# Kernel optimization log

Measured on AMD Instinct MI355X. Metric: run time of the kernel, lower is better.

Reference implementation:

```python
import jax, jax.numpy as jnp
import numpy as np

B, T, N, FIN, FOUT, EDGE_DIM = 8, 16, 256, 32, 32, 16


def setup_inputs() -> dict:
    key = jax.random.key(0)
    ks = jax.random.split(key, 8)
    def xavier(k, shape):
        fan_in, fan_out = shape[0], shape[1]
        limit = float(np.sqrt(6.0 / (fan_in + fan_out)))
        return jax.random.uniform(k, shape, jnp.float32, -limit, limit)
    return {
        "x": jax.random.normal(ks[0], (B, T, N, FIN), jnp.float32),
        "adj": jax.random.uniform(ks[1], (N, N), jnp.float32),
        # edge_net: Linear(1, edge_dim) -> GELU -> Linear(edge_dim, Fin*Fout)
        "w1": xavier(ks[2], (1, EDGE_DIM)),
        "b1": jnp.zeros((EDGE_DIM,), jnp.float32),
        "w2": xavier(ks[3], (EDGE_DIM, FIN * FOUT)),
        "b2": jnp.zeros((FIN * FOUT,), jnp.float32),
        # node_lin: Linear(Fin, Fout)
        "node_w": xavier(ks[4], (FIN, FOUT)),
        "node_b": jnp.zeros((FOUT,), jnp.float32),
    }


def reference(x, adj, w1, b1, w2, b2, node_w, node_b):
    # edge-conditioned weights: (N, N, Fin, Fout)
    h = jax.nn.gelu(adj[:, :, None] * w1[0] + b1, approximate=False)  # (N,N,E)
    edge_w = (h @ w2 + b2).reshape(N, N, FIN, FOUT)
    # msg[b,t,i,j,:] = sum_f x[b,t,j,f] * edge_w[i,j,f,:]; agg = sum_j msg
    agg = jnp.einsum("btjf,ijfo->btio", x, edge_w)  # (B,T,N,Fout)
    y = jax.nn.gelu(x @ node_w + node_b + agg, approximate=False)
    return y
```

## Files before the change

kernel.cpp:

```cpp
#include <hip/hip_runtime.h>
#include <math.h>

#define NB    256
#define FINN  32
#define FOUTN 32
#define BT    128


typedef __attribute__((ext_vector_type(8))) short short8;
typedef __attribute__((ext_vector_type(4))) float floatx4;

#define MFMA16(a,b,c) __builtin_amdgcn_mfma_f32_16x16x32_bf16((a),(b),(c),0,0,0)

__device__ __forceinline__ float gelu_f(float v) {
    return 0.5f * v * (1.0f + erff(v * 0.70710678118654752f));
}
__device__ __forceinline__ ushort f2bf(float x) {
    union { float f; unsigned u; } v; v.f = x;
    unsigned r = (v.u + 0x7FFFu + ((v.u >> 16) & 1u)) >> 16;
    return (ushort)r;
}
__device__ __forceinline__ uint2 pack4(floatx4 d) {
    uint2 p;
    p.x = (unsigned)f2bf(d[0]) | ((unsigned)f2bf(d[1]) << 16);
    p.y = (unsigned)f2bf(d[2]) | ((unsigned)f2bf(d[3]) << 16);
    return p;
}

typedef __attribute__((address_space(1))) void gvoid_t;
typedef __attribute__((address_space(3))) void lvoid_t;
__device__ __forceinline__ void gload_lds16(const void* g, void* l) {
    __builtin_amdgcn_global_load_lds((gvoid_t*)g, (lvoid_t*)l, 16, 0, 0);
}

__global__ __launch_bounds__(256) void prep_kernel(
        const float* __restrict__ x,   const float* __restrict__ adj,
        const float* __restrict__ w1,  const float* __restrict__ b1,
        const float* __restrict__ w2,  const float* __restrict__ b2,
        const float* __restrict__ node_w, const float* __restrict__ node_b,
        ushort* __restrict__ Hf, ushort* __restrict__ w2f,
        ushort* __restrict__ xaf, ushort* __restrict__ nwf,
        float* __restrict__ bias2g) {
    int bid = blockIdx.x;
    int tid = threadIdx.x;

    if (bid < 128) {
        __shared__ float adjs[16][264];
        __shared__ float w1s[16], b1s[16];
        int it = bid & 15;
        int kq8 = bid >> 4;
        if (tid < 16) { w1s[tid] = w1[tid]; b1s[tid] = b1[tid]; }
        #pragma unroll
        for (int q = 0; q < 4; ++q) {
            int u = q * 256 + tid;
            int row = u >> 6, c4 = u & 63;
            *(float4*)&adjs[row][c4 * 4] =
                ((const float4*)(adj + ((size_t)it * 16 + row) * 256))[c4];
        }
        __syncthreads();
        #pragma unroll
        for (int q = 0; q < 4; ++q) {
            int u = q * 256 + tid;
            int ks = kq8 * 16 + (u >> 6);
            int lane = u & 63;
            int m = lane & 15, quad = lane >> 4;
            int e = ks >> 3;
            int j0 = (ks & 7) * 32 + quad * 8;
            float w = w1s[e], b = b1s[e];
            ushort tmp[8];
            #pragma unroll
            for (int d = 0; d < 8; ++d)
                tmp[d] = f2bf(gelu_f(adjs[m][j0 + d] * w + b));
            *(int4*)(Hf + (((size_t)it * 128 + ks) * 64 + lane) * 8) = *(int4*)tmp;
        }
        return;
    }
    if (bid < 160) {
        int wv = tid >> 6, lane = tid & 63, m = lane & 15, quad = lane >> 4;
        int bt = (bid - 128) * 4 + wv;
        #pragma unroll
        for (int jt = 0; jt < 16; ++jt) {
            const float* xs = x + ((size_t)bt * NB + jt * 16 + m) * FINN + quad * 8;
            float4 lo = *(const float4*)xs;
            float4 hi = *(const float4*)(xs + 4);
            ushort tmp[8];
            tmp[0]=f2bf(lo.x); tmp[1]=f2bf(lo.y); tmp[2]=f2bf(lo.z); tmp[3]=f2bf(lo.w);
            tmp[4]=f2bf(hi.x); tmp[5]=f2bf(hi.y); tmp[6]=f2bf(hi.z); tmp[7]=f2bf(hi.w);
            *(int4*)(xaf + (((size_t)bt * 16 + jt) * 64 + lane) * 8) = *(int4*)tmp;
        }
        return;
    }
    if (bid < 288) {
        __shared__ float Sp[8][32];
        __shared__ float Svs[32];
        int bt = bid - 160;
        int f = tid & 31, grp = tid >> 5;
        float s = 0.f;
        for (int j = grp; j < NB; j += 8)
            s += x[((size_t)bt * NB + j) * FINN + f];
        Sp[grp][f] = s;
        __syncthreads();
        if (tid < 32) {
            float s2 = 0.f;
            #pragma unroll
            for (int g = 0; g < 8; ++g) s2 += Sp[g][tid];
            Svs[tid] = s2;
        }
        __syncthreads();
        if (tid < 32) {
            float bb = node_b[tid];
            #pragma unroll
            for (int f2 = 0; f2 < FINN; ++f2)
                bb += Svs[f2] * b2[f2 * FOUTN + tid];
            bias2g[bt * 32 + tid] = bb;
        }
        return;
    }
    for (int s = 0; s < 2048; s += 256) {
        int slot = s + tid;
        int e = slot >> 7, r = slot & 127;
        int ot = r >> 6, lane = r & 63;
        int m = lane & 15, quad = lane >> 4;
        const float* src = w2 + (size_t)e * 1024 + (quad * 8) * 32 + ot * 16 + m;
        ushort tmp[8];
        #pragma unroll
        for (int i = 0; i < 8; ++i) tmp[i] = f2bf(src[i * 32]);
        *(int4*)(w2f + (size_t)slot * 8) = *(int4*)tmp;
    }
    if (tid < 128) {
        int ot = tid >> 6, lane = tid & 63, m = lane & 15, q = lane >> 4;
        ushort tmp[8];
        #pragma unroll
        for (int d = 0; d < 8; ++d)
            tmp[d] = f2bf(node_w[(q * 8 + d) * 32 + ot * 16 + m]);
        *(int4*)(nwf + tid * 8) = *(int4*)tmp;
    }
}

__global__ __launch_bounds__(512, 1) void main_kernel(
        const ushort* __restrict__ Hf,  const ushort* __restrict__ w2f,
        const ushort* __restrict__ xaf, float* __restrict__ Cp) {
    __shared__ ushort Asl[2][2][16][512];
    __shared__ ushort Bsl[2][2][4][512];

    int btq  = blockIdx.x;
    int oh   = blockIdx.y;
    int kq   = blockIdx.z;
    int tid  = threadIdx.x;
    int wv   = tid >> 6;
    int lane = tid & 63;
    int m    = lane & 15;
    int quad = lane >> 4;

    int pbt = wv & 3;
    int pjh = wv >> 2;
    int btg = btq * 4 + pbt;

    short8 xfr[8];
    #pragma unroll
    for (int p = 0; p < 8; ++p)
        xfr[p] = *(const short8*)(xaf + (((size_t)btg * 16 + p * 2 + pjh) * 64 + lane) * 8);

    floatx4 acc[2][4] = {};

    #define STAGE_A(buf, c)                                                   \
    {                                                                         \
        _Pragma("unroll")                                                     \
        for (int s = 0; s < 4; ++s) {                                         \
            int fid = s * 8 + wv;                    \
            int itA = fid & 15, ksL = fid >> 4;                               \
            int ksg = kq * 32 + (c) * 2 + ksL;                                \
            gload_lds16(Hf + (((size_t)itA * 128 + ksg) * 64 + lane) * 8,     \
                        &Asl[buf][ksL][itA][lane * 8]);                       \
        }                                                                     \
    }
    #define PRODUCE(buf, c)                                                   \
    {                                                                         \
        _Pragma("unroll")                                                     \
        for (int s = 0; s < 2; ++s) {                                         \
            int ksg = kq * 32 + (c) * 2 + s;                                  \
            int e = ksg >> 3, p = ksg & 7;                                    \
            short8 wf = *(const short8*)(w2f + (size_t)e * 1024 + oh * 512 + lane * 8); \
            floatx4 z = {0.f, 0.f, 0.f, 0.f};                                 \
            floatx4 d = MFMA16(xfr[p], wf, z);                                \
            int qc = pjh * 2 + (quad >> 1), dp = (quad & 1) * 4;              \
            *(uint2*)&Bsl[buf][s][pbt][(qc * 16 + m) * 8 + dp] = pack4(d);    \
        }                                                                     \
    }
    #define GEMMC(buf)                                                        \
    {                                                                         \
        _Pragma("unroll")                                                     \
        for (int kk = 0; kk < 2; ++kk) {                                      \
            short8 a0 = *(const short8*)&Asl[buf][kk][wv * 2 + 0][lane * 8];  \
            short8 a1 = *(const short8*)&Asl[buf][kk][wv * 2 + 1][lane * 8];  \
            _Pragma("unroll")                                                 \
            for (int bb = 0; bb < 4; ++bb) {                                  \
                short8 b = *(const short8*)&Bsl[buf][kk][bb][lane * 8];       \
                acc[0][bb] = MFMA16(a0, b, acc[0][bb]);                       \
                acc[1][bb] = MFMA16(a1, b, acc[1][bb]);                       \
            }                                                                 \
        }                                                                     \
    }

    STAGE_A(0, 0);
    PRODUCE(0, 0);
    __syncthreads();
    #pragma unroll
    for (int c = 0; c < 16; ++c) {
        if (c < 15) {
            STAGE_A((c + 1) & 1, c + 1);
            PRODUCE((c + 1) & 1, c + 1);
        }
        GEMMC(c & 1);
        __syncthreads();
    }

    #pragma unroll
    for (int t = 0; t < 2; ++t) {
        #pragma unroll
        for (int bb = 0; bb < 4; ++bb) {
            #pragma unroll
            for (int r = 0; r < 4; ++r) {
                int i = (wv * 2 + t) * 16 + quad * 4 + r;
                Cp[(((size_t)kq * BT + btq * 4 + bb) * NB + i) * FOUTN + oh * 16 + m]
                    = acc[t][bb][r];
            }
        }
    }
    #undef STAGE_A
    #undef PRODUCE
    #undef GEMMC
}

__global__ __launch_bounds__(256) void epi_kernel(
        const ushort* __restrict__ xaf, const ushort* __restrict__ nwf,
        const float* __restrict__ bias2g, const float* __restrict__ Cp,
        float* __restrict__ out) {
    int bt   = blockIdx.x;
    int tid  = threadIdx.x;
    int wv   = tid >> 6;
    int lane = tid & 63;
    int m    = lane & 15;
    int quad = lane >> 4;

    short8 nb0 = *(const short8*)(nwf + (size_t)lane * 8);
    short8 nb1 = *(const short8*)(nwf + ((size_t)64 + lane) * 8);

    #pragma unroll
    for (int t = 0; t < 4; ++t) {
        int it = wv * 4 + t;
        short8 xa = *(const short8*)(xaf + (((size_t)bt * 16 + it) * 64 + lane) * 8);
        #pragma unroll
        for (int tn = 0; tn < 2; ++tn) {
            floatx4 z = {0.f, 0.f, 0.f, 0.f};
            floatx4 ea = MFMA16(xa, tn ? nb1 : nb0, z);
            float bz = bias2g[bt * 32 + tn * 16 + m];
            #pragma unroll
            for (int r = 0; r < 4; ++r) {
                int i = it * 16 + quad * 4 + r;
                float s = ea[r] + bz;
                #pragma unroll
                for (int kqi = 0; kqi < 4; ++kqi)
                    s += Cp[(((size_t)kqi * BT + bt) * NB + i) * FOUTN + tn * 16 + m];
                out[((size_t)bt * NB + i) * FOUTN + tn * 16 + m] = gelu_f(s);
            }
        }
    }
}

extern "C" void kernel_launch(void* const* d_in, const int* in_sizes, int n_in,
                              void* d_out, int out_size, void* d_ws, size_t ws_size,
                              hipStream_t stream) {
    const float* x      = (const float*)d_in[0];
    const float* adj    = (const float*)d_in[1];
    const float* w1     = (const float*)d_in[2];
    const float* b1     = (const float*)d_in[3];
    const float* w2     = (const float*)d_in[4];
    const float* b2     = (const float*)d_in[5];
    const float* node_w = (const float*)d_in[6];
    const float* node_b = (const float*)d_in[7];
    float* out = (float*)d_out;

    ushort* Hf     = (ushort*)d_ws;
    ushort* w2f    = Hf + (size_t)16 * 128 * 512;
    ushort* xaf    = w2f + 16384;
    ushort* nwf    = xaf + (size_t)128 * 16 * 512;
    float*  bias2g = (float*)(nwf + 1024);
    float*  Cp     = bias2g + 128 * 32;

    hipLaunchKernelGGL(prep_kernel, dim3(289), dim3(256), 0, stream,
                       x, adj, w1, b1, w2, b2, node_w, node_b,
                       Hf, w2f, xaf, nwf, bias2g);
    hipLaunchKernelGGL(main_kernel, dim3(32, 2, 4), dim3(512), 0, stream,
                       Hf, w2f, xaf, Cp);
    hipLaunchKernelGGL(epi_kernel, dim3(BT), dim3(256), 0, stream,
                       xaf, nwf, bias2g, Cp, out);
}
```

Before: 113.9 us.

## Restructure main GEMM grid per bt with register-streamed A operand

Changes the main kernel decomposition from (btq, output half, k-quarter) blocks to one block per (bt, k-quarter) that covers both output halves. The H operand is now double-buffered in registers straight from global memory instead of being staged through LDS with async global-to-LDS loads, and the w2 fragments are held in registers for the whole block. Launch bounds now allow four blocks per CU, and the barrier becomes a custom lgkmcnt wait plus s_barrier. The aim is higher occupancy and fewer LDS round trips, at the cost of more global reads of H per block and less reuse of H across bt.

Result: faster. 109.9 us (-3.5%).

```diff
diff --git a/kernel.cpp b/kernel.cpp
--- a/kernel.cpp
+++ b/kernel.cpp
@@ -12,6 +12,8 @@
 
 #define MFMA16(a,b,c) __builtin_amdgcn_mfma_f32_16x16x32_bf16((a),(b),(c),0,0,0)
 
+#define BARRIER() asm volatile("s_waitcnt lgkmcnt(0)\n\ts_barrier" ::: "memory")
+
 __device__ __forceinline__ float gelu_f(float v) {
     return 0.5f * v * (1.0f + erff(v * 0.70710678118654752f));
 }
@@ -19,18 +21,15 @@
     union { float f; unsigned u; } v; v.f = x;
     unsigned r = (v.u + 0x7FFFu + ((v.u >> 16) & 1u)) >> 16;
     return (ushort)r;
+}
+__device__ __forceinline__ float bf2f(ushort b) {
+    union { unsigned u; float f; } v; v.u = ((unsigned)b) << 16; return v.f;
 }
 __device__ __forceinline__ uint2 pack4(floatx4 d) {
     uint2 p;
     p.x = (unsigned)f2bf(d[0]) | ((unsigned)f2bf(d[1]) << 16);
     p.y = (unsigned)f2bf(d[2]) | ((unsigned)f2bf(d[3]) << 16);
     return p;
-}
-
-typedef __attribute__((address_space(1))) void gvoid_t;
-typedef __attribute__((address_space(3))) void lvoid_t;
-__device__ __forceinline__ void gload_lds16(const void* g, void* l) {
-    __builtin_amdgcn_global_load_lds((gvoid_t*)g, (lvoid_t*)l, 16, 0, 0);
 }
 
 __global__ __launch_bounds__(256) void prep_kernel(
@@ -137,97 +136,90 @@
     }
 }
 
-__global__ __launch_bounds__(512, 1) void main_kernel(
+__global__ __launch_bounds__(512, 4) void main_kernel(
         const ushort* __restrict__ Hf,  const ushort* __restrict__ w2f,
         const ushort* __restrict__ xaf, float* __restrict__ Cp) {
-    __shared__ ushort Asl[2][2][16][512];
-    __shared__ ushort Bsl[2][2][4][512];
-
-    int btq  = blockIdx.x;
-    int oh   = blockIdx.y;
-    int kq   = blockIdx.z;
+    __shared__ ushort Bsl[2][8][2][512];
+
+    int bt   = blockIdx.x;
+    int kq   = blockIdx.y;
     int tid  = threadIdx.x;
     int wv   = tid >> 6;
     int lane = tid & 63;
     int m    = lane & 15;
     int quad = lane >> 4;
 
-    int pbt = wv & 3;
-    int pjh = wv >> 2;
-    int btg = btq * 4 + pbt;
-
-    short8 xfr[8];
-    #pragma unroll
-    for (int p = 0; p < 8; ++p)
-        xfr[p] = *(const short8*)(xaf + (((size_t)btg * 16 + p * 2 + pjh) * 64 + lane) * 8);
-
-    floatx4 acc[2][4] = {};
-
-    #define STAGE_A(buf, c)                                                   \
+    short8 xfr[2];
+    #pragma unroll
+    for (int t = 0; t < 2; ++t)
+        xfr[t] = *(const short8*)(xaf + (((size_t)bt * 16 + wv + 8 * t) * 64 + lane) * 8);
+    short8 wfr[4][2];
+    #pragma unroll
+    for (int e_ = 0; e_ < 4; ++e_)
+        #pragma unroll
+        for (int ot = 0; ot < 2; ++ot)
+            wfr[e_][ot] = *(const short8*)(w2f + (size_t)(kq * 4 + e_) * 1024
+                                           + ot * 512 + lane * 8);
+
+    short8 areg[2][2];
+    floatx4 acc[2][2] = {};
+
+    #define ALOADS(pp, s_)                                                    \
+    {                                                                         \
+        int ks_ = kq * 32 + (s_);                                             \
+        areg[pp][0] = *(const short8*)(Hf + (((size_t)(2 * wv + 0) * 128 + ks_) * 64 + lane) * 8); \
+        areg[pp][1] = *(const short8*)(Hf + (((size_t)(2 * wv + 1) * 128 + ks_) * 64 + lane) * 8); \
+    }
+    #define PRODUCE(buf, w_)                                                  \
+    {                                                                         \
+        int qc = (wv & 1) * 2 + (quad >> 1);                                  \
+        int dp = (quad & 1) * 4;                                              \
+        _Pragma("unroll")                                                     \
+        for (int t = 0; t < 2; ++t) {                                         \
+            int jp = (wv >> 1) + 4 * t;                                       \
+            floatx4 z = {0.f, 0.f, 0.f, 0.f};                                 \
+            floatx4 d0 = MFMA16(xfr[t], wfr[w_][0], z);                       \
+            floatx4 d1 = MFMA16(xfr[t], wfr[w_][1], z);                       \
+            *(uint2*)&Bsl[buf][jp][0][(qc * 16 + m) * 8 + dp] = pack4(d0);    \
+            *(uint2*)&Bsl[buf][jp][1][(qc * 16 + m) * 8 + dp] = pack4(d1);    \
+        }                                                                     \
+    }
+    #define GEMMC(buf, w_)                                                    \
     {                                                                         \
         _Pragma("unroll")                                                     \
-        for (int s = 0; s < 4; ++s) {                                         \
-            int fid = s * 8 + wv;                    \
-            int itA = fid & 15, ksL = fid >> 4;                               \
-            int ksg = kq * 32 + (c) * 2 + ksL;                                \
-            gload_lds16(Hf + (((size_t)itA * 128 + ksg) * 64 + lane) * 8,     \
-                        &Asl[buf][ksL][itA][lane * 8]);                       \
+        for (int kk = 0; kk < 8; ++kk) {                                      \
+            int s = (w_) * 8 + kk;                                            \
+            if (s < 31) ALOADS((s + 1) & 1, s + 1);                           \
+            short8 b0 = *(const short8*)&Bsl[buf][kk][0][lane * 8];           \
+            short8 b1 = *(const short8*)&Bsl[buf][kk][1][lane * 8];           \
+            acc[0][0] = MFMA16(areg[s & 1][0], b0, acc[0][0]);                \
+            acc[0][1] = MFMA16(areg[s & 1][0], b1, acc[0][1]);                \
+            acc[1][0] = MFMA16(areg[s & 1][1], b0, acc[1][0]);                \
+            acc[1][1] = MFMA16(areg[s & 1][1], b1, acc[1][1]);                \
         }                                                                     \
     }
-    #define PRODUCE(buf, c)                                                   \
-    {                                                                         \
-        _Pragma("unroll")                                                     \
-        for (int s = 0; s < 2; ++s) {                                         \
-            int ksg = kq * 32 + (c) * 2 + s;                                  \
-            int e = ksg >> 3, p = ksg & 7;                                    \
-            short8 wf = *(const short8*)(w2f + (size_t)e * 1024 + oh * 512 + lane * 8); \
-            floatx4 z = {0.f, 0.f, 0.f, 0.f};                                 \
-            floatx4 d = MFMA16(xfr[p], wf, z);                                \
-            int qc = pjh * 2 + (quad >> 1), dp = (quad & 1) * 4;              \
-            *(uint2*)&Bsl[buf][s][pbt][(qc * 16 + m) * 8 + dp] = pack4(d);    \
-        }                                                                     \
-    }
-    #define GEMMC(buf)                                                        \
-    {                                                                         \
-        _Pragma("unroll")                                                     \
-        for (int kk = 0; kk < 2; ++kk) {                                      \
-            short8 a0 = *(const short8*)&Asl[buf][kk][wv * 2 + 0][lane * 8];  \
-            short8 a1 = *(const short8*)&Asl[buf][kk][wv * 2 + 1][lane * 8];  \
-            _Pragma("unroll")                                                 \
-            for (int bb = 0; bb < 4; ++bb) {                                  \
-                short8 b = *(const short8*)&Bsl[buf][kk][bb][lane * 8];       \
-                acc[0][bb] = MFMA16(a0, b, acc[0][bb]);                       \
-                acc[1][bb] = MFMA16(a1, b, acc[1][bb]);                       \
-            }                                                                 \
-        }                                                                     \
-    }
-
-    STAGE_A(0, 0);
+
+    ALOADS(0, 0);
     PRODUCE(0, 0);
-    __syncthreads();
-    #pragma unroll
-    for (int c = 0; c < 16; ++c) {
-        if (c < 15) {
-            STAGE_A((c + 1) & 1, c + 1);
-            PRODUCE((c + 1) & 1, c + 1);
-        }
-        GEMMC(c & 1);
-        __syncthreads();
-    }
-
-    #pragma unroll
-    for (int t = 0; t < 2; ++t) {
-        #pragma unroll
-        for (int bb = 0; bb < 4; ++bb) {
+    BARRIER();
+    #pragma unroll
+    for (int w = 0; w < 4; ++w) {
+        if (w < 3) PRODUCE((w + 1) & 1, w + 1);
+        GEMMC(w & 1, w);
+        BARRIER();
+    }
+
+    #pragma unroll
+    for (int t = 0; t < 2; ++t)
+        #pragma unroll
+        for (int oh = 0; oh < 2; ++oh)
             #pragma unroll
             for (int r = 0; r < 4; ++r) {
-                int i = (wv * 2 + t) * 16 + quad * 4 + r;
-                Cp[(((size_t)kq * BT + btq * 4 + bb) * NB + i) * FOUTN + oh * 16 + m]
-                    = acc[t][bb][r];
+                int i = (2 * wv + t) * 16 + quad * 4 + r;
+                Cp[(((size_t)kq * BT + bt) * NB + i) * FOUTN + oh * 16 + m]
+                    = acc[t][oh][r];
             }
-        }
-    }
-    #undef STAGE_A
+    #undef ALOADS
     #undef PRODUCE
     #undef GEMMC
 }
@@ -291,7 +283,7 @@
     hipLaunchKernelGGL(prep_kernel, dim3(289), dim3(256), 0, stream,
                        x, adj, w1, b1, w2, b2, node_w, node_b,
                        Hf, w2f, xaf, nwf, bias2g);
-    hipLaunchKernelGGL(main_kernel, dim3(32, 2, 4), dim3(512), 0, stream,
+    hipLaunchKernelGGL(main_kernel, dim3(BT, 4), dim3(512), 0, stream,
                        Hf, w2f, xaf, Cp);
     hipLaunchKernelGGL(epi_kernel, dim3(BT), dim3(256), 0, stream,
                        xaf, nwf, bias2g, Cp, out);
```
